# Kernel tuning notes

Hardware: AMD Instinct MI355X
Metric: run time of the kernel (lower is better)

## Reference

```python
import jax, jax.numpy as jnp
import numpy as np

N = 8192
D = 512
N_SLICE = 64
K = 8
H = 30 * K  # 240


def _gen_k_slice(rng):
    xx = rng.normal(0.0, 1.0, (N_SLICE, K, D))
    slices = np.zeros((N_SLICE, K, D), dtype=np.float64)
    for i in range(N_SLICE):
        _, _, vh = np.linalg.svd(xx[i], full_matrices=False)
        slices[i] = vh
    return slices.astype(np.float32)


def setup_inputs() -> dict:
    key = jax.random.key(0)
    k1, k2, k3, k4, k5, k6, k7 = jax.random.split(key, 7)
    rng = np.random.default_rng(0)
    # conv weights: PyTorch Conv1d default init ~ U(-s, s), s = 1/sqrt(fan_in)
    s1 = 1.0 / np.sqrt(K)
    s3 = 1.0 / np.sqrt(H)
    return {
        "X": jax.random.normal(k1, (N, D), dtype=jnp.float32),
        "Y": jax.random.normal(k2, (N, D), dtype=jnp.float32),
        "X_noise": jax.random.normal(k3, (N, N_SLICE * K), dtype=jnp.float32),
        "thetas": jnp.asarray(_gen_k_slice(rng)),                     # [S, K, D]
        "W1": jax.random.uniform(k4, (N_SLICE, H, K), jnp.float32, -s1, s1),
        "b1": jax.random.uniform(k5, (N_SLICE, H), jnp.float32, -s1, s1),
        "W3": jax.random.uniform(k6, (N_SLICE, H), jnp.float32, -s3, s3),
        "b3": jax.random.uniform(k7, (N_SLICE,), jnp.float32, -s3, s3),
        "sigma_noise": 0,
    }


def _mlp(sample, W1, b1, W3, b3):
    # sample: [N, S, K] -> grouped 1x1 conv k->H, relu, grouped conv H->1
    h1 = jax.nn.relu(jnp.einsum('nsk,shk->nsh', sample, W1) + b1[None])
    return jnp.einsum('nsh,sh->ns', h1, W3) + b3[None]  # [N, S]


def reference(X, Y, X_noise, thetas, W1, b1, W3, b3, sigma_noise):
    # batched per-slice projections (fuses the n_slice matmul loop)
    x_sample = jnp.einsum('nd,skd->nsk', X, thetas)  # [N, S, K]
    y_sample = jnp.einsum('nd,skd->nsk', Y, thetas)
    if sigma_noise > 0:
        x_sample = x_sample + sigma_noise * X_noise.reshape(X.shape[0], N_SLICE, K)
    pred_x = _mlp(x_sample, W1, b1, W3, b3)  # [N, S]
    pred_y = _mlp(y_sample, W1, b1, W3, b3)
    n_y = pred_y.shape[0]
    ret = jnp.mean(pred_x, axis=0) - jax.nn.logsumexp(
        pred_y - jnp.log(jnp.float32(n_y)), axis=0)
    return jnp.mean(-ret)
```

## Files before the change

### kernel.cpp

```cpp
#include <hip/hip_runtime.h>
#include <hip/hip_bf16.h>

#define NROWS 8192
#define DDIM  512
#define NS    64
#define KK    8
#define HH    240
#define SP    136
#define BOFFU 4096
#define STGU  8192
#define BWOFF 8704

typedef __attribute__((ext_vector_type(8))) _Float16 f16x8;
typedef __attribute__((ext_vector_type(4))) _Float16 f16x4;
typedef __attribute__((ext_vector_type(4))) float f32x4;

typedef __attribute__((address_space(3))) void       lds_void;
typedef const __attribute__((address_space(1))) void gbl_cvoid;

__device__ inline unsigned pk2u(float a, float b) {
    auto h = __builtin_amdgcn_cvt_pkrtz(a, b);
    unsigned u;
    __builtin_memcpy(&u, &h, sizeof(u));
    return u;
}

__device__ inline f16x4 pk4(float a, float b, float c, float d) {
    uint2 u = make_uint2(pk2u(a, b), pk2u(c, d));
    f16x4 r;
    __builtin_memcpy(&r, &u, sizeof(r));
    return r;
}

__device__ inline void gl16(const ushort* g, ushort* l) {
    __builtin_amdgcn_global_load_lds((gbl_cvoid*)g, (lds_void*)l, 16, 0, 0);
}
__device__ inline void glf(const float* g, ushort* l) {
    __builtin_amdgcn_global_load_lds((gbl_cvoid*)g, (lds_void*)l, 16, 0, 0);
}

__global__ __launch_bounds__(256)
void pack_kernel(const float* __restrict__ Th, const float* __restrict__ W1,
                 const float* __restrict__ b1, const float* __restrict__ W3,
                 ushort* __restrict__ Thh, ushort* __restrict__ W1h,
                 ushort* __restrict__ bwh)
{
    int t = blockIdx.x * 256 + threadIdx.x;
    if (t < 65536) {
        int i = t * 4;
        float4 v = *(const float4*)(Th + i);
        *(uint2*)(Thh + i) = make_uint2(pk2u(v.x, v.y), pk2u(v.z, v.w));
    } else if (t < 96256) {
        int i = (t - 65536) * 4;
        float4 v = *(const float4*)(W1 + i);
        *(uint2*)(W1h + i) = make_uint2(pk2u(v.x, v.y), pk2u(v.z, v.w));
    } else {
        int j = t - 96256;
        int s = j / 60, r = j % 60;
        int src = s * HH + (r >> 2) * 16 + (r & 3) * 4;
        float4 b4 = *(const float4*)(b1 + src);
        float4 w4 = *(const float4*)(W3 + src);
        uint4 o = make_uint4(pk2u(b4.x, b4.y), pk2u(b4.z, b4.w),
                             pk2u(w4.x, w4.y), pk2u(w4.z, w4.w));
        *(uint4*)(bwh + j * 8) = o;
    }
}

__global__ __launch_bounds__(256, 4)
void proj_mlp_kernel(const float* __restrict__ X,
                     const float* __restrict__ Y,
                     const float* __restrict__ Xn,
                     const ushort* __restrict__ Thh,
                     const ushort* __restrict__ W1h,
                     const ushort* __restrict__ bwh,
                     const float* __restrict__ sig_p,
                     float* __restrict__ sumx,
                     float* __restrict__ maxy,
                     float* __restrict__ sey)
{
    __shared__ __align__(16) ushort smem[16384];
    ushort* sl = smem;

    const int tid  = threadIdx.x;
    const int w    = __builtin_amdgcn_readfirstlane(tid >> 6);
    const int lane = tid & 63;
    const int bx   = blockIdx.x;
    const int by   = blockIdx.y;

    const bool isX = (bx < 128);
    const int  bxl = isX ? bx : (bx - 128);
    const float*  srcA = (isX ? X : Y) + (size_t)bxl * 64 * DDIM;
    const ushort* srcB = Thh + (size_t)by * 128 * DDIM;

    const int arow = (w << 4) + (lane >> 2);
    const int asw  = (arow >> 1) & 3;
    const float* gA0 = srcA + (size_t)arow * DDIM + (((lane & 3) ^ asw) + 0) * 4;
    const float* gA1 = srcA + (size_t)arow * DDIM + (((lane & 3) ^ asw) + 4) * 4;

    const int grow = (w << 4) + (lane >> 2);
    const int gchk = (lane & 3) ^ ((grow >> 1) & 3);
    const ushort* gB0 = srcB + (size_t)grow * DDIM + gchk * 8;
    const ushort* gB1 = srcB + (size_t)(grow + 64) * DDIM + gchk * 8;
    const int woff = w * 512;

#define ISSUE(kf, stU) { const int k_ = (kf) * 32; ushort* s_ = smem + (stU); \
    glf(gA0 + k_, s_ + w * 1024); \
    glf(gA1 + k_, s_ + w * 1024 + 512); \
    gl16(gB0 + k_, s_ + BOFFU + woff); \
    gl16(gB1 + k_, s_ + BOFFU + 2048 + woff); }

    f32x4 acc[2][4];
#pragma unroll
    for (int m = 0; m < 2; ++m)
#pragma unroll
        for (int n = 0; n < 4; ++n) acc[m][n] = (f32x4){0.f, 0.f, 0.f, 0.f};

    const int wr  = (w >> 1) * 32;
    const int wc  = (w & 1) * 64;
    const int r16 = lane & 15;
    const int hi4 = lane >> 4;

    int offA32[2][2];
#pragma unroll
    for (int m = 0; m < 2; ++m) {
        int row = wr + m * 16 + r16;
        int sw  = (row >> 1) & 3;
#pragma unroll
        for (int cc = 0; cc < 2; ++cc) {
            int c = hi4 * 2 + cc;
            int p = (c & 4) | ((c & 3) ^ sw);
            offA32[m][cc] = (row >> 4) * 2048 + (p >> 2) * 1024
                          + (row & 15) * 64 + (p & 3) * 16;
        }
    }
    int offB[4];
#pragma unroll
    for (int n = 0; n < 4; ++n) {
        int row = wc + n * 16 + r16;
        offB[n] = BOFFU + row * 32 + ((hi4 ^ ((row >> 1) & 3)) * 8);
    }

    ISSUE(0, 0);

#pragma unroll
    for (int kt = 0; kt < 16; ++kt) {
        asm volatile("s_waitcnt vmcnt(0)\n\ts_barrier" ::: "memory");

        if (kt < 15) ISSUE(kt + 1, ((kt + 1) & 1) * STGU);

        const int curU = (kt & 1) * STGU;
        const char* curB = (const char*)smem + (kt & 1) * 16384;

        f16x8 af[2], bfv[4];
#pragma unroll
        for (int m = 0; m < 2; ++m) {
            f32x4 lo = *(const f32x4*)(curB + offA32[m][0]);
            f32x4 hi = *(const f32x4*)(curB + offA32[m][1]);
            uint4 u = make_uint4(pk2u(lo[0], lo[1]), pk2u(lo[2], lo[3]),
                                 pk2u(hi[0], hi[1]), pk2u(hi[2], hi[3]));
            __builtin_memcpy(&af[m], &u, 16);
        }
#pragma unroll
        for (int n = 0; n < 4; ++n) bfv[n] = *(const f16x8*)(smem + curU + offB[n]);
#pragma unroll
        for (int m = 0; m < 2; ++m)
#pragma unroll
            for (int n = 0; n < 4; ++n)
                acc[m][n] = __builtin_amdgcn_mfma_f32_16x16x32_f16(
                    af[m], bfv[n], acc[m][n], 0, 0, 0);
    }
    __syncthreads();

    {
        const ushort* g = bwh + (size_t)by * 7680;
#pragma unroll
        for (int r = 0; r < 4; ++r) {
            const int ch = r * 256 + w * 64;
            gl16(g + (size_t)(ch + lane) * 8, smem + BWOFF + ch * 8);
        }
    }

    const float sig = *sig_p;
    const bool addnoise = (sig > 0.f) && isX;
    const int n0g = bxl * 64;

#pragma unroll
    for (int m = 0; m < 2; ++m)
#pragma unroll
        for (int n = 0; n < 4; ++n) {
            const int col  = wc + n * 16 + r16;
            const int rowb = wr + m * 16 + hi4 * 4;
            float v[4];
#pragma unroll
            for (int j = 0; j < 4; ++j) {
                v[j] = acc[m][n][j];
                if (addnoise)
                    v[j] = fmaf(sig, Xn[(size_t)(n0g + rowb + j) * (NS * KK) + by * 128 + col], v[j]);
            }
            unsigned u01 = pk2u(v[0], v[1]);
            unsigned u23 = pk2u(v[2], v[3]);
            sl[(rowb + 0) * SP + col] = (ushort)u01;
            sl[(rowb + 1) * SP + col] = (ushort)(u01 >> 16);
            sl[(rowb + 2) * SP + col] = (ushort)u23;
            sl[(rowb + 3) * SP + col] = (ushort)(u23 >> 16);
        }
    asm volatile("s_waitcnt vmcnt(0)" ::: "memory");
    __syncthreads();

#pragma unroll 1
    for (int si = 0; si < 4; ++si) {
        const int sloc = w * 4 + si;
        const int s    = by * 16 + sloc;

        f16x4 bsamp[4];
#pragma unroll
        for (int nt = 0; nt < 4; ++nt) {
            f16x4 t = {0, 0, 0, 0};
            if (hi4 < 2)
                t = *(const f16x4*)(sl + (nt * 16 + r16) * SP + sloc * 8 + hi4 * 4);
            bsamp[nt] = t;
        }

        const ushort* w1p = W1h + (size_t)s * HH * KK;

        f32x4 acc2[4];
#pragma unroll
        for (int nt = 0; nt < 4; ++nt) acc2[nt] = (f32x4){0.f, 0.f, 0.f, 0.f};

#pragma unroll 5
        for (int ht = 0; ht < HH / 16; ++ht) {
            f16x4 aw = {0, 0, 0, 0};
            if (hi4 < 2)
                aw = *(const f16x4*)(w1p + (ht * 16 + r16) * 8 + hi4 * 4);
            f16x8 bw = *(const f16x8*)(smem + BWOFF + ((sloc * 15 + ht) * 4 + hi4) * 8);
            f32x4 z = (f32x4){(float)bw[0], (float)bw[1], (float)bw[2], (float)bw[3]};
            f16x4 w3f = {bw[4], bw[5], bw[6], bw[7]};
#pragma unroll
            for (int nt = 0; nt < 4; ++nt) {
                f32x4 t = __builtin_amdgcn_mfma_f32_16x16x16f16(aw, bsamp[nt], z, 0, 0, 0);
                f16x4 tb = pk4(fmaxf(t[0], 0.f), fmaxf(t[1], 0.f),
                               fmaxf(t[2], 0.f), fmaxf(t[3], 0.f));
                acc2[nt] = __builtin_amdgcn_mfma_f32_16x16x16f16(w3f, tb, acc2[nt], 0, 0, 0);
            }
        }

        if (isX) {
            float lsum = acc2[0][0] + acc2[1][0] + acc2[2][0] + acc2[3][0];
            lsum += __shfl_xor(lsum, 1);
            lsum += __shfl_xor(lsum, 2);
            lsum += __shfl_xor(lsum, 4);
            lsum += __shfl_xor(lsum, 8);
            if (lane == 0) sumx[s * 128 + bxl] = lsum;
        } else {
            float p[4];
#pragma unroll
            for (int nt = 0; nt < 4; ++nt) p[nt] = acc2[nt][0];
            float M = fmaxf(fmaxf(p[0], p[1]), fmaxf(p[2], p[3]));
            float se = __expf(p[0] - M) + __expf(p[1] - M)
                     + __expf(p[2] - M) + __expf(p[3] - M);
#pragma unroll
            for (int off = 1; off < 16; off <<= 1) {
                float Mo = __shfl_xor(M, off);
                float so = __shfl_xor(se, off);
                float Mm = fmaxf(M, Mo);
                se = se * __expf(M - Mm) + so * __expf(Mo - Mm);
                M = Mm;
            }
            if (lane == 0) {
                maxy[s * 128 + bxl] = M;
                sey[s * 128 + bxl]  = se;
            }
        }
    }
}

__global__ __launch_bounds__(256)
void final_kernel(const float* __restrict__ sumx,
                  const float* __restrict__ maxy,
                  const float* __restrict__ sey,
                  float* __restrict__ out)
{
    __shared__ float term_s[NS];
    const int tid = threadIdx.x;
    const int s = tid >> 2, q = tid & 3;
    const int base = s * 128 + q * 32;

    float4 sx[8], my[8], sev[8];
#pragma unroll
    for (int i = 0; i < 8; ++i) {
        sx[i]  = *(const float4*)(sumx + base + i * 4);
        my[i]  = *(const float4*)(maxy + base + i * 4);
        sev[i] = *(const float4*)(sey + base + i * 4);
    }

    float sum = 0.f, M = -3.4e38f;
#pragma unroll
    for (int i = 0; i < 8; ++i) {
        sum += (sx[i].x + sx[i].y) + (sx[i].z + sx[i].w);
        M = fmaxf(M, fmaxf(fmaxf(my[i].x, my[i].y), fmaxf(my[i].z, my[i].w)));
    }
    float se = 0.f;
#pragma unroll
    for (int i = 0; i < 8; ++i) {
        se += sev[i].x * __expf(my[i].x - M) + sev[i].y * __expf(my[i].y - M)
            + sev[i].z * __expf(my[i].z - M) + sev[i].w * __expf(my[i].w - M);
    }

#pragma unroll
    for (int off = 1; off < 4; off <<= 1) {
        float Mo = __shfl_xor(M, off);
        float so = __shfl_xor(se, off);
        float su = __shfl_xor(sum, off);
        float Mm = fmaxf(M, Mo);
        se = se * __expf(M - Mm) + so * __expf(Mo - Mm);
        M = Mm;
        sum += su;
    }
    if (q == 0)
        term_s[s] = M + logf(se) - logf((float)NROWS) - sum * (1.0f / (float)NROWS);
    __syncthreads();
    if (tid < 64) {
        float v = term_s[tid];
#pragma unroll
        for (int off = 1; off < 64; off <<= 1) v += __shfl_xor(v, off);
        if (tid == 0) out[0] = v * (1.0f / (float)NS);
    }
}

extern "C" void kernel_launch(void* const* d_in, const int* in_sizes, int n_in,
                              void* d_out, int out_size, void* d_ws, size_t ws_size,
                              hipStream_t stream)
{
    const float* X   = (const float*)d_in[0];
    const float* Y   = (const float*)d_in[1];
    const float* Xn  = (const float*)d_in[2];
    const float* Th  = (const float*)d_in[3];
    const float* W1  = (const float*)d_in[4];
    const float* b1  = (const float*)d_in[5];
    const float* W3  = (const float*)d_in[6];
    const float* sig = (const float*)d_in[8];

    ushort* Thh  = (ushort*)d_ws;
    ushort* W1h  = Thh + 262144;
    ushort* bwh  = W1h + 122880;
    float*  sumx = (float*)(bwh + 61440);
    float*  maxy = sumx + NS * 128;
    float*  sey  = maxy + NS * 128;

    pack_kernel<<<391, 256, 0, stream>>>(Th, W1, b1, W3, Thh, W1h, bwh);

    dim3 g1(256, 4, 1);
    proj_mlp_kernel<<<g1, 256, 0, stream>>>(X, Y, Xn, Thh, W1h, bwh,
                                            sig, sumx, maxy, sey);
    final_kernel<<<1, 256, 0, stream>>>(sumx, maxy, sey, (float*)d_out);
}
```

Measured before the change: 64.52 us.

## Load fp32 A tiles straight into registers and prefetch MLP weights early

The fp32 X/Y operand is now read with vector global loads directly into registers in the MFMA fragment layout, prefetched one k-step ahead. This replaces staging it through LDS with swizzled offsets, so only the f16 theta tile is double-buffered in LDS, in a smaller buffer. The goal is to cut LDS traffic and LDS address math per k-step. The packed W1/bias copy into LDS is also issued before the main loop, so it overlaps the projection GEMM rather than following it. In exchange, the two warps that share the same A rows now each fetch them from global memory, and the per-lane global accesses are less coalesced.

```diff
diff --git a/kernel.cpp b/kernel.cpp
--- a/kernel.cpp
+++ b/kernel.cpp
@@ -7,8 +7,7 @@
 #define KK    8
 #define HH    240
 #define SP    136
-#define BOFFU 4096
-#define STGU  8192
+#define BSTG  4096
 #define BWOFF 8704
 
 typedef __attribute__((ext_vector_type(8))) _Float16 f16x8;
@@ -32,10 +31,15 @@
     return r;
 }
 
+__device__ inline f16x8 pk8(float4 lo, float4 hi) {
+    uint4 u = make_uint4(pk2u(lo.x, lo.y), pk2u(lo.z, lo.w),
+                         pk2u(hi.x, hi.y), pk2u(hi.z, hi.w));
+    f16x8 r;
+    __builtin_memcpy(&r, &u, sizeof(r));
+    return r;
+}
+
 __device__ inline void gl16(const ushort* g, ushort* l) {
-    __builtin_amdgcn_global_load_lds((gbl_cvoid*)g, (lds_void*)l, 16, 0, 0);
-}
-__device__ inline void glf(const float* g, ushort* l) {
     __builtin_amdgcn_global_load_lds((gbl_cvoid*)g, (lds_void*)l, 16, 0, 0);
 }
 
@@ -92,10 +96,13 @@
     const float*  srcA = (isX ? X : Y) + (size_t)bxl * 64 * DDIM;
     const ushort* srcB = Thh + (size_t)by * 128 * DDIM;
 
-    const int arow = (w << 4) + (lane >> 2);
-    const int asw  = (arow >> 1) & 3;
-    const float* gA0 = srcA + (size_t)arow * DDIM + (((lane & 3) ^ asw) + 0) * 4;
-    const float* gA1 = srcA + (size_t)arow * DDIM + (((lane & 3) ^ asw) + 4) * 4;
+    const int wr  = (w >> 1) * 32;
+    const int wc  = (w & 1) * 64;
+    const int r16 = lane & 15;
+    const int hi4 = lane >> 4;
+
+    const float* gA0 = srcA + (size_t)(wr + r16) * DDIM + hi4 * 8;
+    const float* gA1 = srcA + (size_t)(wr + 16 + r16) * DDIM + hi4 * 8;
 
     const int grow = (w << 4) + (lane >> 2);
     const int gchk = (lane & 3) ^ ((grow >> 1) & 3);
@@ -103,11 +110,13 @@
     const ushort* gB1 = srcB + (size_t)(grow + 64) * DDIM + gchk * 8;
     const int woff = w * 512;
 
-#define ISSUE(kf, stU) { const int k_ = (kf) * 32; ushort* s_ = smem + (stU); \
-    glf(gA0 + k_, s_ + w * 1024); \
-    glf(gA1 + k_, s_ + w * 1024 + 512); \
-    gl16(gB0 + k_, s_ + BOFFU + woff); \
-    gl16(gB1 + k_, s_ + BOFFU + 2048 + woff); }
+    float4 ra0, ra1, ra2, ra3;
+#define LOADA(kf) { const int kA = (kf) * 32; \
+    ra0 = *(const float4*)(gA0 + kA);      ra1 = *(const float4*)(gA0 + kA + 4); \
+    ra2 = *(const float4*)(gA1 + kA);      ra3 = *(const float4*)(gA1 + kA + 4); }
+#define ISSUEB(kf, stU) { const int k_ = (kf) * 32; ushort* s_ = smem + (stU); \
+    gl16(gB0 + k_, s_ + woff); \
+    gl16(gB1 + k_, s_ + 2048 + woff); }
 
     f32x4 acc[2][4];
 #pragma unroll
@@ -115,53 +124,42 @@
 #pragma unroll
         for (int n = 0; n < 4; ++n) acc[m][n] = (f32x4){0.f, 0.f, 0.f, 0.f};
 
-    const int wr  = (w >> 1) * 32;
-    const int wc  = (w & 1) * 64;
-    const int r16 = lane & 15;
-    const int hi4 = lane >> 4;
-
-    int offA32[2][2];
-#pragma unroll
-    for (int m = 0; m < 2; ++m) {
-        int row = wr + m * 16 + r16;
-        int sw  = (row >> 1) & 3;
-#pragma unroll
-        for (int cc = 0; cc < 2; ++cc) {
-            int c = hi4 * 2 + cc;
-            int p = (c & 4) | ((c & 3) ^ sw);
-            offA32[m][cc] = (row >> 4) * 2048 + (p >> 2) * 1024
-                          + (row & 15) * 64 + (p & 3) * 16;
-        }
-    }
     int offB[4];
 #pragma unroll
     for (int n = 0; n < 4; ++n) {
         int row = wc + n * 16 + r16;
-        offB[n] = BOFFU + row * 32 + ((hi4 ^ ((row >> 1) & 3)) * 8);
-    }
-
-    ISSUE(0, 0);
+        offB[n] = row * 32 + ((hi4 ^ ((row >> 1) & 3)) * 8);
+    }
+
+    LOADA(0);
+    ISSUEB(0, 0);
+    {
+        const ushort* g = bwh + (size_t)by * 7680;
+#pragma unroll
+        for (int r = 0; r < 4; ++r) {
+            const int ch = r * 256 + w * 64;
+            if (ch < 960)
+                gl16(g + (size_t)(ch + lane) * 8, smem + BWOFF + ch * 8);
+        }
+    }
 
 #pragma unroll
     for (int kt = 0; kt < 16; ++kt) {
         asm volatile("s_waitcnt vmcnt(0)\n\ts_barrier" ::: "memory");
 
-        if (kt < 15) ISSUE(kt + 1, ((kt + 1) & 1) * STGU);
-
-        const int curU = (kt & 1) * STGU;
-        const char* curB = (const char*)smem + (kt & 1) * 16384;
-
-        f16x8 af[2], bfv[4];
-#pragma unroll
-        for (int m = 0; m < 2; ++m) {
-            f32x4 lo = *(const f32x4*)(curB + offA32[m][0]);
-            f32x4 hi = *(const f32x4*)(curB + offA32[m][1]);
-            uint4 u = make_uint4(pk2u(lo[0], lo[1]), pk2u(lo[2], lo[3]),
-                                 pk2u(hi[0], hi[1]), pk2u(hi[2], hi[3]));
-            __builtin_memcpy(&af[m], &u, 16);
-        }
-#pragma unroll
-        for (int n = 0; n < 4; ++n) bfv[n] = *(const f16x8*)(smem + curU + offB[n]);
+        f16x8 af[2];
+        af[0] = pk8(ra0, ra1);
+        af[1] = pk8(ra2, ra3);
+
+        if (kt < 15) {
+            ISSUEB(kt + 1, ((kt + 1) & 1) * BSTG);
+            LOADA(kt + 1);
+        }
+
+        const int cur = (kt & 1) * BSTG;
+        f16x8 bfv[4];
+#pragma unroll
+        for (int n = 0; n < 4; ++n) bfv[n] = *(const f16x8*)(smem + cur + offB[n]);
 #pragma unroll
         for (int m = 0; m < 2; ++m)
 #pragma unroll
@@ -170,15 +168,6 @@
                     af[m], bfv[n], acc[m][n], 0, 0, 0);
     }
     __syncthreads();
-
-    {
-        const ushort* g = bwh + (size_t)by * 7680;
-#pragma unroll
-        for (int r = 0; r < 4; ++r) {
-            const int ch = r * 256 + w * 64;
-            gl16(g + (size_t)(ch + lane) * 8, smem + BWOFF + ch * 8);
-        }
-    }
 
     const float sig = *sig_p;
     const bool addnoise = (sig > 0.f) && isX;
@@ -204,7 +193,6 @@
             sl[(rowb + 2) * SP + col] = (ushort)u23;
             sl[(rowb + 3) * SP + col] = (ushort)(u23 >> 16);
         }
-    asm volatile("s_waitcnt vmcnt(0)" ::: "memory");
     __syncthreads();
 
 #pragma unroll 1
```

After: 82.20 us. 1.27x slower.
